# Performance work log

Measured on AMD Instinct MI355X. Metric: run time of the kernel, lower is better.

## Reference

```python
import jax, jax.numpy as jnp
import numpy as np

HID = 1024       # hidden_size
H = 8            # num_attention_heads
KVH = 2          # num_key_value_heads
D = HID // H     # head_dim = 128
WINDOW = 2048    # sliding_window
THETA = 10000.0  # rope_theta
B, S = 1, 4096


def rotate_half(x):
    x1, x2 = jnp.split(x, 2, axis=-1)
    return jnp.concatenate([-x2, x1], axis=-1)


def setup_inputs() -> dict:
    key = jax.random.key(0)
    ks = jax.random.split(key, 5)
    scale = 0.02
    return {
        "hidden_states": jax.random.normal(ks[0], (B, S, HID), dtype=jnp.float32),
        "wq": jax.random.normal(ks[1], (H * D, HID), dtype=jnp.float32) * scale,
        "wk": jax.random.normal(ks[2], (KVH * D, HID), dtype=jnp.float32) * scale,
        "wv": jax.random.normal(ks[3], (KVH * D, HID), dtype=jnp.float32) * scale,
        "wo": jax.random.normal(ks[4], (HID, H * D), dtype=jnp.float32) * scale,
        "position_ids": jnp.broadcast_to(jnp.arange(S, dtype=jnp.int64 if jax.config.jax_enable_x64 else jnp.int32)[None, :], (B, S)),
    }


def reference(hidden_states, wq, wk, wv, wo, position_ids):
    b, s, _ = hidden_states.shape
    # projections (torch nn.Linear: x @ W^T)
    q = (hidden_states @ wq.T).reshape(b, s, H, D).transpose(0, 2, 1, 3)      # bhsd
    k = (hidden_states @ wk.T).reshape(b, s, KVH, D).transpose(0, 2, 1, 3)    # b(kv)sd
    v = (hidden_states @ wv.T).reshape(b, s, KVH, D).transpose(0, 2, 1, 3)

    # RoPE cache (head_dim, seq_len)
    inv_freq = 1.0 / THETA ** (jnp.arange(0, D, 2, dtype=jnp.float32) / D)
    t = jnp.arange(s, dtype=jnp.float32)
    freqs = t[:, None] * inv_freq[None, :]
    emb = jnp.concatenate([freqs, freqs], axis=-1)           # (S, D)
    cos = jnp.cos(emb)[position_ids][:, None]                # (B,1,S,D)
    sin = jnp.sin(emb)[position_ids][:, None]
    q = q * cos + rotate_half(q) * sin
    k = k * cos + rotate_half(k) * sin

    # GQA: repeat kv heads to match query heads (repeat_interleave on head dim)
    groups = H // KVH
    k = jnp.repeat(k, groups, axis=1)
    v = jnp.repeat(v, groups, axis=1)

    # full score matrix with sliding-window causal mask
    scores = jnp.einsum("bhqd,bhkd->bhqk", q, k)
    i = jnp.arange(s)[:, None]
    j = jnp.arange(s)[None, :]
    mask = (j <= i) & (j > i - WINDOW)                       # causal + window
    scores = jnp.where(mask[None, None], scores, -jnp.inf) / jnp.sqrt(jnp.float32(D))

    probs = jax.nn.softmax(scores.astype(jnp.float32), axis=-1).astype(q.dtype)
    ctx = jnp.einsum("bhqk,bhkd->bhqd", probs, v)
    ctx = ctx.transpose(0, 2, 1, 3).reshape(b, s, H * D)
    return ctx @ wo.T
```

## Files before the change

kernel.cpp:

```cpp
#include <hip/hip_runtime.h>

#define S_LEN 4096
#define HIDDEN 1024
#define NH 8
#define NKV 2
#define HD 128
#define WIN 2048

typedef short bf16x8 __attribute__((ext_vector_type(8)));
typedef short bf16x4 __attribute__((ext_vector_type(4)));
typedef float f32x4 __attribute__((ext_vector_type(4)));
typedef unsigned short u16x4 __attribute__((ext_vector_type(4)));

__device__ __forceinline__ unsigned short f2b(float f) {
    unsigned int u = __builtin_bit_cast(unsigned int, f);
    u += 0x7fffu + ((u >> 16) & 1u);
    return (unsigned short)(u >> 16);
}
__device__ __forceinline__ float b2f(unsigned short u) {
    unsigned int x = ((unsigned int)u) << 16;
    return __builtin_bit_cast(float, x);
}

__device__ __forceinline__ void gl_lds16(const unsigned short* g, unsigned short* l) {
    __builtin_amdgcn_global_load_lds(
        (const __attribute__((address_space(1))) unsigned int*)g,
        (__attribute__((address_space(3))) unsigned int*)l, 16, 0, 0);
}

#define WAIT_VM6   0x0F76
#define WAIT_VM0   0x0F70
#define MEMFENCE() __asm__ volatile("" ::: "memory")

__global__ __launch_bounds__(256) void cvt5(
    const float* __restrict__ s0, unsigned short* __restrict__ t0, int n0,
    const float* __restrict__ s1, unsigned short* __restrict__ t1, int n1,
    const float* __restrict__ s2, unsigned short* __restrict__ t2, int n2,
    const float* __restrict__ s3, unsigned short* __restrict__ t3, int n3,
    const float* __restrict__ s4, unsigned short* __restrict__ t4, int n4)
{
    int i = blockIdx.x * 256 + threadIdx.x;
    const float* s; unsigned short* t;
    if (i < n0)              { s = s0; t = t0; }
    else if ((i -= n0) < n1) { s = s1; t = t1; }
    else if ((i -= n1) < n2) { s = s2; t = t2; }
    else if ((i -= n2) < n3) { s = s3; t = t3; }
    else if ((i -= n3) < n4) { s = s4; t = t4; }
    else return;
    f32x4 v = *(const f32x4*)(s + (size_t)i * 4);
    u16x4 r = { f2b(v[0]), f2b(v[1]), f2b(v[2]), f2b(v[3]) };
    *(u16x4*)(t + (size_t)i * 4) = r;
}

__global__ __launch_bounds__(256, 2) void gemm128(
    const unsigned short* __restrict__ A, const unsigned short* __restrict__ W,
    float* __restrict__ Cf, unsigned short* __restrict__ Cb,
    int M, int N, int K)
{
    __shared__ alignas(16) unsigned short As[6][64 * 32];
    __shared__ alignas(16) unsigned short Bs[6][128 * 32];

    int lane = threadIdx.x & 63;
    int w = threadIdx.x >> 6;
    int l15 = lane & 15, quad = lane >> 4;

    int tiles_n = N >> 7;
    int bid = (int)blockIdx.x;
    int nb = (int)gridDim.x;
    int lb = bid;
    if ((nb & 7) == 0) {
        int c = nb >> 3;
        lb = (bid & 7) * c + (bid >> 3);
    }
    int mt0 = lb / tiles_n;
    int nt0 = lb - mt0 * tiles_n;

    size_t goffA;
    {
        int s = w * 64 + lane;
        int row = s >> 2, spos = s & 3;
        int kblk = spos ^ ((row >> 1) & 3);
        goffA = (size_t)(mt0 * 64 + row) * K + kblk * 8;
    }
    size_t goffB[2];
    #pragma unroll
    for (int is = 0; is < 2; ++is) {
        int s = w * 128 + is * 64 + lane;
        int row = s >> 2, spos = s & 3;
        int kblk = spos ^ ((row >> 1) & 3);
        goffB[is] = (size_t)(nt0 * 128 + row) * K + kblk * 8;
    }

    int arow0 = (w >> 1) * 32;
    int brow0 = (w & 1) * 64;
    int aoff[2], boff[4];
    #pragma unroll
    for (int t = 0; t < 2; ++t) {
        int ra = arow0 + t * 16 + l15;
        aoff[t] = (ra * 4 + (quad ^ ((ra >> 1) & 3))) * 8;
    }
    #pragma unroll
    for (int j = 0; j < 4; ++j) {
        int rb = brow0 + j * 16 + l15;
        boff[j] = (rb * 4 + (quad ^ ((rb >> 1) & 3))) * 8;
    }

    f32x4 acc[2][4];
    #pragma unroll
    for (int i = 0; i < 2; ++i)
        #pragma unroll
        for (int j = 0; j < 4; ++j) acc[i][j] = (f32x4){0.f, 0.f, 0.f, 0.f};

    auto stage = [&](int s, int b) {
        int k0 = s * 32;
        gl_lds16(A + goffA + k0, &As[b][(w * 64) * 8]);
        gl_lds16(W + goffB[0] + k0, &Bs[b][(w * 128 + 0) * 8]);
        gl_lds16(W + goffB[1] + k0, &Bs[b][(w * 128 + 64) * 8]);
    };

    int nk = K >> 5;
    int np = nk >> 1;
    if (nk > 0) stage(0, 0);
    if (nk > 1) stage(1, 1);
    if (nk > 2) stage(2, 2);
    if (nk > 3) stage(3, 3);
    int cb = 0, sb = 4;
    for (int j = 0; j < np; ++j) {
        MEMFENCE();
        if (j + 1 < np) __builtin_amdgcn_s_waitcnt(WAIT_VM6);
        else            __builtin_amdgcn_s_waitcnt(WAIT_VM0);
        __builtin_amdgcn_s_barrier();
        MEMFENCE();
        int s0 = 2 * j + 4;
        if (s0 < nk)     stage(s0, sb);
        if (s0 + 1 < nk) stage(s0 + 1, sb + 1 == 6 ? 0 : sb + 1);
        sb += 2; if (sb >= 6) sb -= 6;

        #pragma unroll
        for (int half = 0; half < 2; ++half) {
            const unsigned short* Ab = &As[cb + half][0];
            const unsigned short* Bb = &Bs[cb + half][0];
            bf16x8 af[2], bf_[4];
            #pragma unroll
            for (int t = 0; t < 2; ++t) af[t]  = *(const bf16x8*)(Ab + aoff[t]);
            #pragma unroll
            for (int jj = 0; jj < 4; ++jj) bf_[jj] = *(const bf16x8*)(Bb + boff[jj]);
            __builtin_amdgcn_s_setprio(1);
            #pragma unroll
            for (int i2 = 0; i2 < 2; ++i2)
                #pragma unroll
                for (int jj = 0; jj < 4; ++jj)
                    acc[i2][jj] = __builtin_amdgcn_mfma_f32_16x16x32_bf16(af[i2], bf_[jj], acc[i2][jj], 0, 0, 0);
            __builtin_amdgcn_s_setprio(0);
        }
        cb += 2; if (cb >= 6) cb -= 6;
        MEMFENCE();
    }

    #pragma unroll
    for (int i = 0; i < 2; ++i) {
        int row0 = mt0 * 64 + arow0 + i * 16 + quad * 4;
        #pragma unroll
        for (int j = 0; j < 4; ++j) {
            int col = nt0 * 128 + brow0 + j * 16 + l15;
            if (Cf) {
                #pragma unroll
                for (int reg = 0; reg < 4; ++reg)
                    Cf[(size_t)(row0 + reg) * N + col] = acc[i][j][reg];
            } else {
                #pragma unroll
                for (int reg = 0; reg < 4; ++reg)
                    Cb[(size_t)(row0 + reg) * N + col] = f2b(acc[i][j][reg]);
            }
        }
    }
}

#define QKVW (HIDDEN + 2 * NKV * HD)
__global__ __launch_bounds__(256, 2) void gemmqkv(
    const unsigned short* __restrict__ A, const unsigned short* __restrict__ W,
    const int* __restrict__ pos,
    unsigned short* __restrict__ Qb, unsigned short* __restrict__ Kb,
    unsigned short* __restrict__ Vt)
{
    __shared__ alignas(16) char pool[73728];
    unsigned short (*As)[64 * 32]  = (unsigned short (*)[64 * 32])(pool);
    unsigned short (*Bs)[128 * 32] = (unsigned short (*)[128 * 32])(pool + 24576);
    float (*Ex)[32][68] = (float (*)[32][68])(pool);
    unsigned short* T = (unsigned short*)(pool);

    int lane = threadIdx.x & 63;
    int w = threadIdx.x >> 6;
    int l15 = lane & 15, quad = lane >> 4;

    const int K = HIDDEN;
    int bid = (int)blockIdx.x;
    int lb = (bid & 7) * 96 + (bid >> 3);
    int mt0 = lb / 12;
    int nt0 = lb - mt0 * 12;

    size_t goffA;
    {
        int s = w * 64 + lane;
        int row = s >> 2, spos = s & 3;
        int kblk = spos ^ ((row >> 1) & 3);
        goffA = (size_t)(mt0 * 64 + row) * K + kblk * 8;
    }
    size_t goffB[2];
    #pragma unroll
    for (int is = 0; is < 2; ++is) {
        int s = w * 128 + is * 64 + lane;
        int row = s >> 2, spos = s & 3;
        int kblk = spos ^ ((row >> 1) & 3);
        goffB[is] = (size_t)(nt0 * 128 + row) * K + kblk * 8;
    }

    int arow0 = (w >> 1) * 32;
    int brow0 = (w & 1) * 64;
    int aoff[2], boff[4];
    #pragma unroll
    for (int t = 0; t < 2; ++t) {
        int ra = arow0 + t * 16 + l15;
        aoff[t] = (ra * 4 + (quad ^ ((ra >> 1) & 3))) * 8;
    }
    #pragma unroll
    for (int j = 0; j < 4; ++j) {
        int rb = brow0 + j * 16 + l15;
        boff[j] = (rb * 4 + (quad ^ ((rb >> 1) & 3))) * 8;
    }

    f32x4 acc[2][4];
    #pragma unroll
    for (int i = 0; i < 2; ++i)
        #pragma unroll
        for (int j = 0; j < 4; ++j) acc[i][j] = (f32x4){0.f, 0.f, 0.f, 0.f};

    auto stage = [&](int s, int b) {
        int k0 = s * 32;
        gl_lds16(A + goffA + k0, &As[b][(w * 64) * 8]);
        gl_lds16(W + goffB[0] + k0, &Bs[b][(w * 128 + 0) * 8]);
        gl_lds16(W + goffB[1] + k0, &Bs[b][(w * 128 + 64) * 8]);
    };

    stage(0, 0);
    stage(1, 1);
    stage(2, 2);
    stage(3, 3);
    int cb = 0, sb = 4;
    for (int j = 0; j < 16; ++j) {
        MEMFENCE();
        if (j < 15) __builtin_amdgcn_s_waitcnt(WAIT_VM6);
        else        __builtin_amdgcn_s_waitcnt(WAIT_VM0);
        __builtin_amdgcn_s_barrier();
        MEMFENCE();
        int s0 = 2 * j + 4;
        if (s0 < 32)     stage(s0, sb);
        if (s0 + 1 < 32) stage(s0 + 1, sb + 1 == 6 ? 0 : sb + 1);
        sb += 2; if (sb >= 6) sb -= 6;

        #pragma unroll
        for (int half = 0; half < 2; ++half) {
            const unsigned short* Ab = &As[cb + half][0];
            const unsigned short* Bb = &Bs[cb + half][0];
            bf16x8 af[2], bf_[4];
            #pragma unroll
            for (int t = 0; t < 2; ++t) af[t]  = *(const bf16x8*)(Ab + aoff[t]);
            #pragma unroll
            for (int jj = 0; jj < 4; ++jj) bf_[jj] = *(const bf16x8*)(Bb + boff[jj]);
            __builtin_amdgcn_s_setprio(1);
            #pragma unroll
            for (int i2 = 0; i2 < 2; ++i2)
                #pragma unroll
                for (int jj = 0; jj < 4; ++jj)
                    acc[i2][jj] = __builtin_amdgcn_mfma_f32_16x16x32_bf16(af[i2], bf_[jj], acc[i2][jj], 0, 0, 0);
            __builtin_amdgcn_s_setprio(0);
        }
        cb += 2; if (cb >= 6) cb -= 6;
        MEMFENCE();
    }

    if (nt0 >= 10) {
        int kv = nt0 - 10;
        __syncthreads();
        #pragma unroll
        for (int i = 0; i < 2; ++i) {
            int srow = arow0 + i * 16 + quad * 4;
            #pragma unroll
            for (int j = 0; j < 4; ++j) {
                int d = brow0 + j * 16 + l15;
                #pragma unroll
                for (int reg = 0; reg < 4; ++reg)
                    T[(srow + reg) * 130 + d] = f2b(acc[i][j][reg]);
            }
        }
        __syncthreads();
        int tid = threadIdx.x;
        int dl = tid >> 4;
        int s4 = (tid & 15) * 4;
        #pragma unroll
        for (int it = 0; it < 8; ++it) {
            int d = it * 16 + dl;
            u16x4 v4 = { T[(s4 + 0) * 130 + d], T[(s4 + 1) * 130 + d],
                         T[(s4 + 2) * 130 + d], T[(s4 + 3) * 130 + d] };
            *(u16x4*)(Vt + (size_t)kv * HD * S_LEN + (size_t)d * S_LEN
                      + mt0 * 64 + s4) = v4;
        }
        return;
    }

    bool isQ = (nt0 < 8);
    int kv = nt0 - 8;
    bool is64 = (pos[1] == 0) && (pos[3] == 0);
    const float qscale = 0.08838834764831843f;

    float invf[4];
    #pragma unroll
    for (int j = 0; j < 4; ++j) {
        int d6 = (brow0 + j * 16 + l15) & 63;
        invf[j] = exp2f(-(float)d6 * (13.287712379549449f / 64.0f));
    }

    __syncthreads();
    #pragma unroll
    for (int i = 0; i < 2; ++i)
        #pragma unroll
        for (int j = 0; j < 4; ++j)
            #pragma unroll
            for (int reg = 0; reg < 4; ++reg)
                Ex[w][i * 16 + quad * 4 + reg][j * 16 + l15] = acc[i][j][reg];
    __syncthreads();
    #pragma unroll
    for (int i = 0; i < 2; ++i) {
        #pragma unroll
        for (int reg = 0; reg < 4; ++reg) {
            int s = mt0 * 64 + arow0 + i * 16 + quad * 4 + reg;
            int pv_ = is64 ? pos[2 * s] : pos[s];
            float pf = (float)pv_;
            #pragma unroll
            for (int j = 0; j < 4; ++j) {
                float sn, cs;
                __sincosf(pf * invf[j], &sn, &cs);
                float a  = acc[i][j][reg];
                float pr = Ex[w ^ 1][i * 16 + quad * 4 + reg][j * 16 + l15];
                int d_local = brow0 + j * 16 + l15;
                float outv = (d_local < 64) ? (a * cs - pr * sn) : (a * cs + pr * sn);
                if (isQ) {
                    Qb[(size_t)s * HIDDEN + nt0 * HD + d_local] = f2b(outv * qscale);
                } else {
                    Kb[(size_t)kv * S_LEN * HD + (size_t)s * HD + d_local] = f2b(outv);
                }
            }
        }
    }
}

__global__ __launch_bounds__(256, 2) void attn_coop(
    const unsigned short* __restrict__ Qb, const unsigned short* __restrict__ Kb,
    const unsigned short* __restrict__ Vt, unsigned short* __restrict__ Ctx)
{
    __shared__ alignas(16) unsigned short Klds[2][64 * 128];
    __shared__ alignas(16) unsigned short Vlds[2][128 * 64];

    int lane = threadIdx.x & 63;
    int w = threadIdx.x >> 6;
    int l15 = lane & 15, quad = lane >> 4;
    int h = blockIdx.y;
    int kv = h >> 2;
    int qt = (h & 4) ? (63 - (int)blockIdx.x) : (int)blockIdx.x;
    int qb = qt * 64;
    int q16 = qb + w * 16;

    bf16x8 a_q[4];
    const unsigned short* qrow = Qb + (size_t)(q16 + l15) * HIDDEN + h * HD + quad * 8;
    #pragma unroll
    for (int st = 0; st < 4; ++st) a_q[st] = *(const bf16x8*)(qrow + st * 32);

    bf16x4 ones4;
    #pragma unroll
    for (int i = 0; i < 4; ++i) ones4[i] = (short)0x3F80;

    int lo = qb - (WIN - 1); if (lo < 0) lo = 0; lo &= ~63;
    int nch = (qb + 64 - lo) >> 6;

    const unsigned short* gbase;
    unsigned short* ldsdst[2];
    int myoff[8];
    int jmul;
    if (w < 2) {
        gbase = Kb + (size_t)kv * S_LEN * HD;
        ldsdst[0] = &Klds[0][w * 8 * 512];
        ldsdst[1] = &Klds[1][w * 8 * 512];
        jmul = HD;
        #pragma unroll
        for (int tt = 0; tt < 8; ++tt) {
            int t = w * 8 + tt;
            int key  = t * 4 + (lane >> 4);
            int dblk = (lane & 15) ^ (key & 15);
            myoff[tt] = key * HD + dblk * 8;
        }
    } else {
        gbase = Vt + (size_t)kv * HD * S_LEN;
        ldsdst[0] = &Vlds[0][(w - 2) * 8 * 512];
        ldsdst[1] = &Vlds[1][(w - 2) * 8 * 512];
        jmul = 1;
        #pragma unroll
        for (int tt = 0; tt < 8; ++tt) {
            int t = (w - 2) * 8 + tt;
            int d    = t * 8 + (lane >> 3);
            int kblk = (lane & 7) ^ (d & 7);
            myoff[tt] = d * S_LEN + kblk * 8;
        }
    }

    auto issue = [&](int c) {
        int j0 = lo + c * 64;
        const unsigned short* src = gbase + (size_t)j0 * jmul;
        unsigned short* dst = ldsdst[c & 1];
        #pragma unroll
        for (int tt = 0; tt < 8; ++tt)
            gl_lds16(src + myoff[tt], dst + tt * 512);
    };

    f32x4 o[9];
    #pragma unroll
    for (int nd = 0; nd < 9; ++nd) o[nd] = (f32x4){0.f, 0.f, 0.f, 0.f};

    issue(0);

    for (int c = 0; c < nch; ++c) {
        int j0 = lo + c * 64;

        MEMFENCE();
        __builtin_amdgcn_s_waitcnt(WAIT_VM0);
        __builtin_amdgcn_s_barrier();
        MEMFENCE();
        if (c + 1 < nch) issue(c + 1);

        const unsigned short* Kc = &Klds[c & 1][0];
        const unsigned short* Vc = &Vlds[c & 1][0];

        f32x4 sc[4];
        #pragma unroll
        for (int t = 0; t < 4; ++t) {
            sc[t] = (f32x4){0.f, 0.f, 0.f, 0.f};
            int key = t * 16 + l15;
            #pragma unroll
            for (int st = 0; st < 4; ++st) {
                int off16 = key * 16 + ((st * 4 + quad) ^ (key & 15));
                bf16x8 ak = *(const bf16x8*)(Kc + off16 * 8);
                sc[t] = __builtin_amdgcn_mfma_f32_16x16x32_bf16(ak, a_q[st], sc[t], 0, 0, 0);
            }
        }

        float p[4][4];
        if (j0 + 63 <= q16 && j0 > q16 + 15 - WIN) {
            #pragma unroll
            for (int t = 0; t < 4; ++t)
                #pragma unroll
                for (int reg = 0; reg < 4; ++reg) p[t][reg] = __expf(sc[t][reg]);
        } else {
            int iq = q16 + l15;
            #pragma unroll
            for (int t = 0; t < 4; ++t) {
                #pragma unroll
                for (int reg = 0; reg < 4; ++reg) {
                    int key = j0 + t * 16 + quad * 4 + reg;
                    p[t][reg] = (key <= iq && key > iq - WIN) ? __expf(sc[t][reg]) : 0.f;
                }
            }
        }

        bf16x4 a_p[4];
        #pragma unroll
        for (int t = 0; t < 4; ++t) {
            a_p[t][0] = (short)f2b(p[t][0]);
            a_p[t][1] = (short)f2b(p[t][1]);
            a_p[t][2] = (short)f2b(p[t][2]);
            a_p[t][3] = (short)f2b(p[t][3]);
        }

        #pragma unroll
        for (int t = 0; t < 4; ++t) {
            #pragma unroll
            for (int nd = 0; nd < 8; ++nd) {
                int d = nd * 16 + l15;
                int kblk = t * 2 + (quad >> 1);
                int slot = d * 8 + (kblk ^ (d & 7));
                bf16x4 bv = *(const bf16x4*)(Vc + slot * 8 + (quad & 1) * 4);
                o[nd] = __builtin_amdgcn_mfma_f32_16x16x16bf16_1k(a_p[t], bv, o[nd], 0, 0, 0);
            }
            o[8] = __builtin_amdgcn_mfma_f32_16x16x16bf16_1k(a_p[t], ones4, o[8], 0, 0, 0);
        }
        MEMFENCE();
    }

    #pragma unroll
    for (int nd = 0; nd < 8; ++nd) {
        int d = nd * 16 + l15;
        #pragma unroll
        for (int reg = 0; reg < 4; ++reg) {
            int q = q16 + quad * 4 + reg;
            Ctx[(size_t)q * HIDDEN + h * HD + d] = f2b(o[nd][reg] / o[8][reg]);
        }
    }
}

extern "C" void kernel_launch(void* const* d_in, const int* in_sizes, int n_in,
                              void* d_out, int out_size, void* d_ws, size_t ws_size,
                              hipStream_t stream)
{
    const float* hidden = (const float*)d_in[0];
    const float* wq = (const float*)d_in[1];
    const float* wk = (const float*)d_in[2];
    const float* wv = (const float*)d_in[3];
    const float* wo = (const float*)d_in[4];
    const int* pos = (const int*)d_in[5];
    float* out = (float*)d_out;

    char* ws = (char*)d_ws;
    size_t off = 0;
    unsigned short* Hb   = (unsigned short*)(ws + off); off += (size_t)S_LEN * HIDDEN * 2;
    unsigned short* Wqkv = (unsigned short*)(ws + off); off += (size_t)QKVW * HIDDEN * 2;
    unsigned short* Wob  = (unsigned short*)(ws + off); off += (size_t)HIDDEN * HIDDEN * 2;
    unsigned short* Qb   = (unsigned short*)(ws + off); off += (size_t)S_LEN * HIDDEN * 2;
    unsigned short* Kb   = (unsigned short*)(ws + off); off += (size_t)S_LEN * NKV * HD * 2;
    unsigned short* Vt   = (unsigned short*)(ws + off); off += (size_t)S_LEN * NKV * HD * 2;
    unsigned short* Cb   = (unsigned short*)(ws + off); off += (size_t)S_LEN * HIDDEN * 2;

    const int n_h  = S_LEN * HIDDEN / 4;
    const int n_wq = HIDDEN * HIDDEN / 4;
    const int n_wk = NKV * HD * HIDDEN / 4;
    int tot4 = n_h + n_wq + 2 * n_wk + n_wq;
    cvt5<<<(tot4 + 255) / 256, 256, 0, stream>>>(
        hidden, Hb, n_h,
        wq, Wqkv, n_wq,
        wk, Wqkv + (size_t)HIDDEN * HIDDEN, n_wk,
        wv, Wqkv + (size_t)(HIDDEN + NKV * HD) * HIDDEN, n_wk,
        wo, Wob, n_wq);

    gemmqkv<<<(S_LEN / 64) * 12, 256, 0, stream>>>(
        Hb, Wqkv, pos, Qb, Kb, Vt);

    attn_coop<<<dim3(S_LEN / 64, NH), 256, 0, stream>>>(Qb, Kb, Vt, Cb);

    gemm128<<<(S_LEN / 64) * (HIDDEN / 128), 256, 0, stream>>>(
        Cb, Wob, out, nullptr, S_LEN, HIDDEN, HIDDEN);
}
```

Baseline: 180.2 us.

## Split long attention query tiles across two blocks with atomic-counter merge

Query tiles whose key range spans more than 17 chunks are split into two halves along a new grid z dimension. Each half writes unnormalized partial outputs and row sums to a workspace, and the second finisher, found with an atomic counter, combines them and writes the context. This evens out per-block work and adds parallelism for the 512-block attention grid, at the cost of extra global traffic, a memset, and launching blocks that exit at once. The merge adds the two partials directly without max rescaling, which works only because the original kernel already skips max subtraction.

```diff
diff --git a/kernel.cpp b/kernel.cpp
--- a/kernel.cpp
+++ b/kernel.cpp
@@ -31,6 +31,8 @@
 #define WAIT_VM6   0x0F76
 #define WAIT_VM0   0x0F70
 #define MEMFENCE() __asm__ volatile("" ::: "memory")
+
+#define NSPLIT_QT 47
 
 __global__ __launch_bounds__(256) void cvt5(
     const float* __restrict__ s0, unsigned short* __restrict__ t0, int n0,
@@ -356,20 +358,31 @@
 
 __global__ __launch_bounds__(256, 2) void attn_coop(
     const unsigned short* __restrict__ Qb, const unsigned short* __restrict__ Kb,
-    const unsigned short* __restrict__ Vt, unsigned short* __restrict__ Ctx)
+    const unsigned short* __restrict__ Vt, unsigned short* __restrict__ Ctx,
+    float* __restrict__ Po, float* __restrict__ Pl, unsigned int* __restrict__ cnt)
 {
     __shared__ alignas(16) unsigned short Klds[2][64 * 128];
     __shared__ alignas(16) unsigned short Vlds[2][128 * 64];
+    __shared__ unsigned int oldv;
 
     int lane = threadIdx.x & 63;
     int w = threadIdx.x >> 6;
     int l15 = lane & 15, quad = lane >> 4;
     int h = blockIdx.y;
+    int z = (int)blockIdx.z;
     int kv = h >> 2;
     int qt = (h & 4) ? (63 - (int)blockIdx.x) : (int)blockIdx.x;
     int qb = qt * 64;
     int q16 = qb + w * 16;
 
+    int lo = qb - (WIN - 1); if (lo < 0) lo = 0; lo &= ~63;
+    int nch = (qb + 64 - lo) >> 6;
+
+    bool split = nch > 17;
+    if (!split && z) return;
+    int cbeg = (split && z) ? (nch >> 1) : 0;
+    int cend = (split && !z) ? (nch >> 1) : nch;
+
     bf16x8 a_q[4];
     const unsigned short* qrow = Qb + (size_t)(q16 + l15) * HIDDEN + h * HD + quad * 8;
     #pragma unroll
@@ -378,9 +391,6 @@
     bf16x4 ones4;
     #pragma unroll
     for (int i = 0; i < 4; ++i) ones4[i] = (short)0x3F80;
-
-    int lo = qb - (WIN - 1); if (lo < 0) lo = 0; lo &= ~63;
-    int nch = (qb + 64 - lo) >> 6;
 
     const unsigned short* gbase;
     unsigned short* ldsdst[2];
@@ -425,16 +435,16 @@
     #pragma unroll
     for (int nd = 0; nd < 9; ++nd) o[nd] = (f32x4){0.f, 0.f, 0.f, 0.f};
 
-    issue(0);
-
-    for (int c = 0; c < nch; ++c) {
+    issue(cbeg);
+
+    for (int c = cbeg; c < cend; ++c) {
         int j0 = lo + c * 64;
 
         MEMFENCE();
         __builtin_amdgcn_s_waitcnt(WAIT_VM0);
         __builtin_amdgcn_s_barrier();
         MEMFENCE();
-        if (c + 1 < nch) issue(c + 1);
+        if (c + 1 < cend) issue(c + 1);
 
         const unsigned short* Kc = &Klds[c & 1][0];
         const unsigned short* Vc = &Vlds[c & 1][0];
@@ -494,13 +504,64 @@
         MEMFENCE();
     }
 
+    if (!split) {
+        #pragma unroll
+        for (int nd = 0; nd < 8; ++nd) {
+            int d = nd * 16 + l15;
+            #pragma unroll
+            for (int reg = 0; reg < 4; ++reg) {
+                int q = q16 + quad * 4 + reg;
+                Ctx[(size_t)q * HIDDEN + h * HD + d] = f2b(o[nd][reg] / o[8][reg]);
+            }
+        }
+        return;
+    }
+
+    int pidx = (qt - 17) * 8 + h;
+    size_t mybase = (size_t)(pidx * 2 + z) * 64;
     #pragma unroll
     for (int nd = 0; nd < 8; ++nd) {
         int d = nd * 16 + l15;
         #pragma unroll
         for (int reg = 0; reg < 4; ++reg) {
+            int ql = w * 16 + quad * 4 + reg;
+            Po[(mybase + ql) * 128 + d] = o[nd][reg];
+        }
+    }
+    if (l15 == 0) {
+        #pragma unroll
+        for (int reg = 0; reg < 4; ++reg) {
+            int ql = w * 16 + quad * 4 + reg;
+            Pl[mybase + ql] = o[8][reg];
+        }
+    }
+    __syncthreads();
+    if (threadIdx.x == 0) {
+        __threadfence();
+        oldv = atomicAdd(&cnt[pidx], 1u);
+    }
+    __syncthreads();
+    if (oldv == 0) return;
+    if (threadIdx.x == 0) __threadfence();
+    __syncthreads();
+
+    size_t pbase = (size_t)(pidx * 2 + (z ^ 1)) * 64;
+    float lp[4];
+    #pragma unroll
+    for (int reg = 0; reg < 4; ++reg) {
+        int ql = w * 16 + quad * 4 + reg;
+        lp[reg] = Pl[pbase + ql];
+    }
+    #pragma unroll
+    for (int nd = 0; nd < 8; ++nd) {
+        int d = nd * 16 + l15;
+        #pragma unroll
+        for (int reg = 0; reg < 4; ++reg) {
+            int ql = w * 16 + quad * 4 + reg;
+            float po = Po[(pbase + ql) * 128 + d];
             int q = q16 + quad * 4 + reg;
-            Ctx[(size_t)q * HIDDEN + h * HD + d] = f2b(o[nd][reg] / o[8][reg]);
+            Ctx[(size_t)q * HIDDEN + h * HD + d] =
+                f2b((o[nd][reg] + po) / (o[8][reg] + lp[reg]));
         }
     }
 }
@@ -526,6 +587,11 @@
     unsigned short* Kb   = (unsigned short*)(ws + off); off += (size_t)S_LEN * NKV * HD * 2;
     unsigned short* Vt   = (unsigned short*)(ws + off); off += (size_t)S_LEN * NKV * HD * 2;
     unsigned short* Cb   = (unsigned short*)(ws + off); off += (size_t)S_LEN * HIDDEN * 2;
+    float* Po            = (float*)(ws + off);          off += (size_t)NSPLIT_QT * 8 * 2 * 64 * 128 * 4;
+    float* Pl            = (float*)(ws + off);          off += (size_t)NSPLIT_QT * 8 * 2 * 64 * 4;
+    unsigned int* cnt    = (unsigned int*)(ws + off);   off += 2048;
+
+    hipMemsetAsync(cnt, 0, NSPLIT_QT * 8 * sizeof(unsigned int), stream);
 
     const int n_h  = S_LEN * HIDDEN / 4;
     const int n_wq = HIDDEN * HIDDEN / 4;
@@ -541,7 +607,8 @@
     gemmqkv<<<(S_LEN / 64) * 12, 256, 0, stream>>>(
         Hb, Wqkv, pos, Qb, Kb, Vt);
 
-    attn_coop<<<dim3(S_LEN / 64, NH), 256, 0, stream>>>(Qb, Kb, Vt, Cb);
+    attn_coop<<<dim3(S_LEN / 64, NH, 2), 256, 0, stream>>>(
+        Qb, Kb, Vt, Cb, Po, Pl, cnt);
 
     gemm128<<<(S_LEN / 64) * (HIDDEN / 128), 256, 0, stream>>>(
         Cb, Wob, out, nullptr, S_LEN, HIDDEN, HIDDEN);
```

New measurement: 212.4 us. +17.9%, slower.
